# Optimization experiments

Hardware: AMD Instinct MI355X
Metric: run time of the kernel (lower is better)

The kernel has to match this reference:

```python
import jax, jax.numpy as jnp
import numpy as np

T = 2048      # time steps (X.shape[0])
D = 64        # input_dim (= future_dim)
H = 1024      # hidden_dim
OUT = 64      # output_dim
ND = 3        # num_decoders


def setup_inputs() -> dict:
    key = jax.random.key(0)
    ks = jax.random.split(key, 20)
    def p(k, shape, scale=0.03):
        return jax.random.normal(k, shape, dtype=jnp.float32) * scale
    return {
        "X": jax.random.normal(ks[0], (T, D), dtype=jnp.float32),
        # enc LSTMCell: input = fusion_dim = 2*D
        "enc_Wih": p(ks[1], (4 * H, 2 * D)), "enc_Whh": p(ks[2], (4 * H, H)),
        "enc_bih": p(ks[3], (4 * H,)), "enc_bhh": p(ks[4], (4 * H,)),
        # dec LSTMCell: input = H
        "dec_Wih": p(ks[5], (4 * H, H)), "dec_Whh": p(ks[6], (4 * H, H)),
        "dec_bih": p(ks[7], (4 * H,)), "dec_bhh": p(ks[8], (4 * H,)),
        # fc_relu heads
        "hx_W": p(ks[9], (H, H)), "hx_b": p(ks[10], (H,)),
        "cx_W": p(ks[11], (H, H)), "cx_b": p(ks[12], (H,)),
        "fus_W": p(ks[13], (H, OUT)), "fus_b": p(ks[14], (H,)),
        "fut_W": p(ks[15], (D, H)), "fut_b": p(ks[16], (D,)),
        # classifier (shared by encoder and decoder)
        "cls_W": p(ks[17], (OUT, H)), "cls_b": p(ks[18], (OUT,)),
    }


def _lstm_cell(x, h, c, Wih, Whh, bih, bhh):
    # torch.nn.LSTMCell gate order: i, f, g, o
    g = x @ Wih.T + bih + h @ Whh.T + bhh
    i, f, gg, o = jnp.split(g, 4, axis=-1)
    c_new = jax.nn.sigmoid(f) * c + jax.nn.sigmoid(i) * jnp.tanh(gg)
    h_new = jax.nn.sigmoid(o) * jnp.tanh(c_new)
    return h_new, c_new


def reference(X, enc_Wih, enc_Whh, enc_bih, enc_bhh,
              dec_Wih, dec_Whh, dec_bih, dec_bhh,
              hx_W, hx_b, cx_W, cx_b, fus_W, fus_b,
              fut_W, fut_b, cls_W, cls_b):
    relu = jax.nn.relu

    def step(carry, x_t):
        enc_hx, enc_cx, fut = carry  # [H], [H], [D]
        fusion = jnp.concatenate([x_t, fut])  # [2D]
        enc_hx, enc_cx = _lstm_cell(fusion, enc_hx, enc_cx,
                                    enc_Wih, enc_Whh, enc_bih, enc_bhh)
        enc_score = enc_hx @ cls_W.T + cls_b  # [OUT]
        dhx = relu(enc_hx @ hx_W.T + hx_b)
        dcx = relu(enc_cx @ cx_W.T + cx_b)
        fusion_in = jnp.zeros((H,), X.dtype)
        fut_new = jnp.zeros((D,), X.dtype)
        dscores = []
        for _ in range(ND):
            # Original bug preserved: decoder returns the UNCHANGED cx
            # (`decc_cx` typo), so dcx is never updated inside this loop.
            dhx, _unused_cx = _lstm_cell(fusion_in, dhx, dcx,
                                         dec_Wih, dec_Whh, dec_bih, dec_bhh)
            ds = dhx @ cls_W.T + cls_b
            dscores.append(ds)
            fusion_in = relu(ds @ fus_W.T + fus_b)
            fut_new = fut_new + relu(dhx @ fut_W.T + fut_b)
        fut_new = fut_new / ND
        return (enc_hx, enc_cx, fut_new), (enc_score, jnp.stack(dscores))

    init = (jnp.zeros((H,), X.dtype), jnp.zeros((H,), X.dtype),
            jnp.zeros((D,), X.dtype))
    _, (enc_scores, dec_scores) = jax.lax.scan(step, init, X[: T - ND])
    # enc_scores: [T-ND, OUT]; dec_scores: [T-ND, ND, OUT] -> [(T-ND)*ND, OUT]
    return enc_scores, dec_scores.reshape(-1, OUT)
```

## Files before the change

### kernel.cpp

```cpp
#include <hip/hip_runtime.h>
#include <hip/hip_bf16.h>


typedef unsigned short u16t;
typedef unsigned int u32t;
typedef unsigned long long u64t;

#define TSTEPS 2045
#define NWG 256
#define NTHR 512
#define SPINCAP 8192

#define HENC  0
#define CENC  4096
#define DHX   8192
#define DD1   12288
#define DD2   16384
#define SFF   20480
#define PARTF 22016

struct Params {
  const void *X, *eWih, *eWhh, *ebih, *ebhh, *dWih, *dWhh, *dbih, *dbhh,
             *hxW, *hxb, *cxW, *cxb, *fusW, *fusb_g, *futW, *futb_g, *clsW, *clsb_g;
  float* ws;
  void* out;
};

struct SharedMem {
  alignas(16) float encW[16 * 1152];
  alignas(16) u16t  decW[16 * 2048];
  alignas(16) float xs[2048];
  float cls_sl[256], fut_sl[256];
  float clsb[64], futb[64], fut_acc[64], dsbuf[64], fv3[64];
  float bias_e[16], bias_d[16], g16[16];
  float h4[4], dcx_s[4], encc[4], hxb4[4], cxb4[4];
  int bail;
  int badcnt;
};

__device__ __forceinline__ float bfu(u16t u){
  union { u32t i; float f; } v; v.i = ((u32t)u) << 16; return v.f;
}
__device__ __forceinline__ u32t fbits(float f){
  union { float f; u32t u; } c; c.f = f; return c.u;
}
__device__ __forceinline__ u16t bf16bits(float v){
  __hip_bfloat16 b = __float2bfloat16(v);
  union { __hip_bfloat16 b; u16t u; } c; c.b = b; return c.u;
}
template<bool F32>
__device__ __forceinline__ float ldE(const void* p, int i){
  if (F32) return ((const float*)p)[i];
  return bfu(((const u16t*)p)[i]);
}
template<bool F32>
__device__ __forceinline__ u16t ldB(const void* p, int i){
  if (F32) return bf16bits(((const float*)p)[i]);
  return ((const u16t*)p)[i];
}
template<bool F32>
__device__ __forceinline__ void stO(void* p, int i, float v){
  if (F32) ((float*)p)[i] = v;
  else     ((u16t*)p)[i] = bf16bits(v);
}
__device__ __forceinline__ float sigm(float x){ return 1.f / (1.f + __expf(-x)); }
__device__ __forceinline__ float tanhx(float x){
  float e = __expf(-2.f * fabsf(x));
  float t = (1.f - e) / (1.f + e);
  return copysignf(t, x);
}
__device__ __forceinline__ void stp(float* rowbase, int idx, float v, u32t ep){
  u64t u = (u64t)fbits(v) | ((u64t)ep << 32);
  __hip_atomic_store((u64t*)rowbase + idx, u,
                     __ATOMIC_RELAXED, __HIP_MEMORY_SCOPE_AGENT);
}
__device__ __forceinline__ float4 ld4c(const float* p){
  float4 r;
  asm volatile("global_load_dwordx4 %0, %1, off sc0 sc1\n\t"
               "s_waitcnt vmcnt(0)"
               : "=&v"(r) : "v"(p) : "memory");
  return r;
}
__device__ __forceinline__ void ld4c4(const float* p0, const float* p1,
                                      const float* p2, const float* p3,
                                      float4& r0, float4& r1, float4& r2, float4& r3){
  asm volatile(
    "global_load_dwordx4 %0, %4, off sc0 sc1\n\t"
    "global_load_dwordx4 %1, %5, off sc0 sc1\n\t"
    "global_load_dwordx4 %2, %6, off sc0 sc1\n\t"
    "global_load_dwordx4 %3, %7, off sc0 sc1\n\t"
    "s_waitcnt vmcnt(0)"
    : "=&v"(r0), "=&v"(r1), "=&v"(r2), "=&v"(r3)
    : "v"(p0), "v"(p1), "v"(p2), "v"(p3)
    : "memory");
}
__device__ __forceinline__ float2 poll2(const float* q, u32t ep, int* bail){
  float4 r; int sp = 0;
  for (;;){
    r = ld4c(q);
    if (fbits(r.y) == ep && fbits(r.w) == ep) break;
    if (*bail) break;
    if (++sp > SPINCAP){ *bail = 1; break; }
  }
  return float2{r.x, r.z};
}

template<bool F32>
__device__ __forceinline__ float hw_dot(const void* wbase, long off,
                                        const float* __restrict__ x,
                                        int K, int lane){
  float acc = 0.f;
  if (F32){
    const float* w = (const float*)wbase + off;
    for (int c = lane * 4; c < K; c += 128){
      float4 wv = *(const float4*)(w + c);
      float4 xv = *(const float4*)(x + c);
      acc = fmaf(wv.x, xv.x, acc); acc = fmaf(wv.y, xv.y, acc);
      acc = fmaf(wv.z, xv.z, acc); acc = fmaf(wv.w, xv.w, acc);
    }
  } else {
    const u16t* w = (const u16t*)wbase + off;
    for (int c = lane * 4; c < K; c += 128){
      ushort4 wv = *(const ushort4*)(w + c);
      float4  xv = *(const float4*)(x + c);
      acc = fmaf(bfu(wv.x), xv.x, acc); acc = fmaf(bfu(wv.y), xv.y, acc);
      acc = fmaf(bfu(wv.z), xv.z, acc); acc = fmaf(bfu(wv.w), xv.w, acc);
    }
  }
  #pragma unroll
  for (int o = 16; o; o >>= 1) acc += __shfl_xor(acc, o, 64);
  return acc;
}

__device__ __forceinline__ float lds_dot_f32(const float* __restrict__ w,
                                             const float* __restrict__ x,
                                             int K, int lane){
  float acc = 0.f;
  for (int c = lane * 4; c < K; c += 128){
    float4 wv = *(const float4*)(w + c);
    float4 xv = *(const float4*)(x + c);
    acc = fmaf(wv.x, xv.x, acc); acc = fmaf(wv.y, xv.y, acc);
    acc = fmaf(wv.z, xv.z, acc); acc = fmaf(wv.w, xv.w, acc);
  }
  #pragma unroll
  for (int o = 16; o; o >>= 1) acc += __shfl_xor(acc, o, 64);
  return acc;
}

__device__ __forceinline__ float lds_dot_bf16(const u16t* __restrict__ w,
                                              const float* __restrict__ x,
                                              int K, int lane){
  float acc = 0.f;
  for (int c = lane * 8; c < K; c += 256){
    uint4  wv = *(const uint4*)(w + c);
    float4 x0 = *(const float4*)(x + c);
    float4 x1 = *(const float4*)(x + c + 4);
    acc = fmaf(bfu((u16t)(wv.x & 0xffff)), x0.x, acc);
    acc = fmaf(bfu((u16t)(wv.x >> 16)),    x0.y, acc);
    acc = fmaf(bfu((u16t)(wv.y & 0xffff)), x0.z, acc);
    acc = fmaf(bfu((u16t)(wv.y >> 16)),    x0.w, acc);
    acc = fmaf(bfu((u16t)(wv.z & 0xffff)), x1.x, acc);
    acc = fmaf(bfu((u16t)(wv.z >> 16)),    x1.y, acc);
    acc = fmaf(bfu((u16t)(wv.w & 0xffff)), x1.z, acc);
    acc = fmaf(bfu((u16t)(wv.w >> 16)),    x1.w, acc);
  }
  #pragma unroll
  for (int o = 16; o; o >>= 1) acc += __shfl_xor(acc, o, 64);
  return acc;
}

template<bool F32>
__device__ __forceinline__ void reduce_phase(float* ws, int ph, int par, u32t ep,
                                             int t, SharedMem& S, void* out,
                                             int w, int hw, int lane){
  const int o = (w & 7) * 16 + hw;
  const float* row = ws + PARTF + (size_t)((par * 3 + ph) * 128 + o) * 512;
  const float* q = row + lane * 16;
  float4 r0, r1, r2, r3; int sp = 0;
  for (;;){
    ld4c4(q, q + 4, q + 8, q + 12, r0, r1, r2, r3);
    if (fbits(r0.y) == ep && fbits(r0.w) == ep && fbits(r1.y) == ep &&
        fbits(r1.w) == ep && fbits(r2.y) == ep && fbits(r2.w) == ep &&
        fbits(r3.y) == ep && fbits(r3.w) == ep) break;
    if (S.bail) break;
    if (++sp > SPINCAP){ S.bail = 1; break; }
  }
  float s = r0.x + r0.z + r1.x + r1.z + r2.x + r2.z + r3.x + r3.z;
  #pragma unroll
  for (int m = 16; m; m >>= 1) s += __shfl_xor(s, m, 64);
  if (lane == 0){
    float* sf = ws + SFF + (par * 3 + ph) * 256;
    if (o < 64){
      float v = s + S.clsb[o];
      stO<F32>(out, TSTEPS * 64 + (t * 3 + ph) * 64 + o, v);
      if (ph < 2) stp(sf, o, v, ep);
    } else {
      float v = fmaxf(s + S.futb[o - 64], 0.f);
      stp(sf, o, v, ep);
    }
  }
}

template<bool F32>
__device__ void run(const Params& p, SharedMem& S){
  const int tid  = threadIdx.x;
  const int w    = blockIdx.x;
  const int hw   = tid >> 5;
  const int lane = tid & 31;
  const long grow = (long)((hw >> 2) * 1024 + 4 * w + (hw & 3));
  float* ws = p.ws;

  {
    float* er = S.encW + hw * 1152;
    for (int c = lane; c < 128; c += 32)  er[c]       = ldE<F32>(p.eWih, (int)(grow * 128 + c));
    for (int c = lane; c < 1024; c += 32) er[128 + c] = ldE<F32>(p.eWhh, (int)(grow * 1024 + c));
    u16t* dr = S.decW + hw * 2048;
    for (int c = lane; c < 1024; c += 32){
      dr[c]        = ldB<F32>(p.dWih, (int)(grow * 1024 + c));
      dr[1024 + c] = ldB<F32>(p.dWhh, (int)(grow * 1024 + c));
    }
  }
  u32t fw[64];
  float fusb0, fusb1;
  {
    int h0 = 2 * tid, h1 = 2 * tid + 1;
    #pragma unroll
    for (int o = 0; o < 64; ++o){
      u16t lo = ldB<F32>(p.fusW, h0 * 64 + o);
      u16t hi = ldB<F32>(p.fusW, h1 * 64 + o);
      fw[o] = ((u32t)hi << 16) | lo;
    }
    fusb0 = ldE<F32>(p.fusb_g, h0);
    fusb1 = ldE<F32>(p.fusb_g, h1);
  }
  if (tid < 256){
    int o = tid >> 2, j = tid & 3;
    S.cls_sl[tid] = ldE<F32>(p.clsW, o * 1024 + 4 * w + j);
    S.fut_sl[tid] = ldE<F32>(p.futW, o * 1024 + 4 * w + j);
  }
  if (tid < 64){
    S.clsb[tid] = ldE<F32>(p.clsb_g, tid);
    S.futb[tid] = ldE<F32>(p.futb_g, tid);
    S.fut_acc[tid] = 0.f;
  }
  if (tid < 16){
    int gr = (tid >> 2) * 1024 + 4 * w + (tid & 3);
    S.bias_e[tid] = ldE<F32>(p.ebih, gr) + ldE<F32>(p.ebhh, gr);
    S.bias_d[tid] = ldE<F32>(p.dbih, gr) + ldE<F32>(p.dbhh, gr);
  }
  if (tid < 4){
    S.hxb4[tid] = ldE<F32>(p.hxb, 4 * w + tid);
    S.cxb4[tid] = ldE<F32>(p.cxb, 4 * w + tid);
    S.encc[tid] = 0.f;
  }
  __syncthreads();

  for (int t = 0; t < TSTEPS; ++t){
    const int  par  = t & 1;
    const int  ppar = par ^ 1;
    const u32t ep   = (u32t)(t + 1);
    const u32t epv  = (u32t)t;

    if (t > 0){
      if (tid < 32){
        const float* base = ws + SFF + (ppar * 3 + 2) * 256;
        float2 v = poll2(base + (32 + tid) * 4, epv, &S.bail);
        S.fv3[2 * tid] = v.x; S.fv3[2 * tid + 1] = v.y;
      }
      float2 v = poll2(ws + HENC + ppar * 2048 + tid * 4, epv, &S.bail);
      S.xs[128 + 2 * tid] = v.x; S.xs[129 + 2 * tid] = v.y;
    } else {
      S.xs[128 + 2 * tid] = 0.f; S.xs[129 + 2 * tid] = 0.f;
    }
    __syncthreads();
    if (tid < 64){
      S.xs[tid] = ldE<F32>(p.X, t * 64 + tid);
      float fv = (t > 0) ? (S.fut_acc[tid] + S.fv3[tid]) * (1.f / 3.f) : 0.f;
      S.xs[64 + tid] = fv;
      S.fut_acc[tid] = 0.f;
    }
    __syncthreads();
    {
      float a = lds_dot_f32(S.encW + hw * 1152, S.xs, 1152, lane) + S.bias_e[hw];
      if (lane == 0) S.g16[hw] = a;
    }
    __syncthreads();
    if (tid < 4){
      float gi = sigm(S.g16[tid]), gf = sigm(S.g16[4 + tid]),
            gg = tanhx(S.g16[8 + tid]), go = sigm(S.g16[12 + tid]);
      float c = gf * S.encc[tid] + gi * gg;
      float h = go * tanhx(c);
      S.encc[tid] = c;
      stp(ws + HENC + par * 2048, 4 * w + tid, h, ep);
      stp(ws + CENC + par * 2048, 4 * w + tid, c, ep);
    }

    {
      float2 v = poll2(ws + HENC + par * 2048 + tid * 4, ep, &S.bail);
      S.xs[2 * tid] = v.x; S.xs[2 * tid + 1] = v.y;
      float2 c = poll2(ws + CENC + par * 2048 + tid * 4, ep, &S.bail);
      S.xs[1024 + 2 * tid] = c.x; S.xs[1025 + 2 * tid] = c.y;
    }
    __syncthreads();
    if (hw < 4){
      float d = fmaxf(hw_dot<F32>(p.hxW, (long)(4 * w + hw) * 1024, S.xs, 1024, lane)
                      + S.hxb4[hw], 0.f);
      if (lane == 0) stp(ws + DHX + par * 2048, 4 * w + hw, d, ep);
    } else if (hw < 8){
      int j = hw - 4;
      float d = fmaxf(hw_dot<F32>(p.cxW, (long)(4 * w + j) * 1024, S.xs + 1024, 1024, lane)
                      + S.cxb4[j], 0.f);
      if (lane == 0) S.dcx_s[j] = d;
    } else if (w >= 8 && w < 16){
      int r = (w - 8) * 8 + (hw - 8);
      float s = hw_dot<F32>(p.clsW, (long)r * 1024, S.xs, 1024, lane) + S.clsb[r];
      if (lane == 0) stO<F32>(p.out, t * 64 + r, s);
    }

    {
      float2 v = poll2(ws + DHX + par * 2048 + tid * 4, ep, &S.bail);
      S.xs[2 * tid] = v.x; S.xs[2 * tid + 1] = v.y;
    }
    __syncthreads();
    {
      float a = lds_dot_bf16(S.decW + hw * 2048 + 1024, S.xs, 1024, lane) + S.bias_d[hw];
      if (lane == 0) S.g16[hw] = a;
    }
    __syncthreads();
    if (tid < 4){
      float gi = sigm(S.g16[tid]), gf = sigm(S.g16[4 + tid]),
            gg = tanhx(S.g16[8 + tid]), go = sigm(S.g16[12 + tid]);
      float c = gf * S.dcx_s[tid] + gi * gg;
      float h = go * tanhx(c);
      S.h4[tid] = h;
      stp(ws + DD1 + par * 2048, 4 * w + tid, h, ep);
    }
    __syncthreads();
    if (tid < 64){
      float sv = 0.f, fv = 0.f;
      #pragma unroll
      for (int j = 0; j < 4; ++j){
        sv = fmaf(S.cls_sl[tid * 4 + j], S.h4[j], sv);
        fv = fmaf(S.fut_sl[tid * 4 + j], S.h4[j], fv);
      }
      float* base = ws + PARTF + (size_t)((par * 3 + 0) * 128) * 512;
      stp(base + (size_t)tid * 512,        w, sv, ep);
      stp(base + (size_t)(64 + tid) * 512, w, fv, ep);
    }

    for (int di = 2; di <= 3; ++di){
      const int ph = di - 2;
      if (w >= 16 + ph * 8 && w < 24 + ph * 8)
        reduce_phase<F32>(ws, ph, par, ep, t, S, p.out, w, hw, lane);
      {
        const float* dbuf = ws + (di == 2 ? DD1 : DD2) + par * 2048;
        float2 v = poll2(dbuf + tid * 4, ep, &S.bail);
        S.xs[1024 + 2 * tid] = v.x; S.xs[1025 + 2 * tid] = v.y;
      }
      __syncthreads();
      float accA = lds_dot_bf16(S.decW + hw * 2048 + 1024, S.xs + 1024, 1024, lane);
      if (tid < 64){
        const float* sf = ws + SFF + (par * 3 + ph) * 256;
        float2 v = poll2(sf + tid * 4, ep, &S.bail);
        if (tid < 32){ S.dsbuf[2 * tid] = v.x; S.dsbuf[2 * tid + 1] = v.y; }
        else { S.fv3[2 * (tid - 32)] = v.x; S.fv3[2 * (tid - 32) + 1] = v.y; }
      }
      __syncthreads();
      if (tid < 64) S.fut_acc[tid] += S.fv3[tid];
      {
        float a0 = fusb0, a1 = fusb1;
        #pragma unroll
        for (int o = 0; o < 64; ++o){
          float d = S.dsbuf[o];
          a0 = fmaf(bfu((u16t)(fw[o] & 0xffff)), d, a0);
          a1 = fmaf(bfu((u16t)(fw[o] >> 16)),    d, a1);
        }
        S.xs[2 * tid]     = fmaxf(a0, 0.f);
        S.xs[2 * tid + 1] = fmaxf(a1, 0.f);
      }
      __syncthreads();
      float accB = lds_dot_bf16(S.decW + hw * 2048, S.xs, 1024, lane);
      {
        float a = accA + accB + S.bias_d[hw];
        if (lane == 0) S.g16[hw] = a;
      }
      __syncthreads();
      if (tid < 4){
        float gi = sigm(S.g16[tid]), gf = sigm(S.g16[4 + tid]),
              gg = tanhx(S.g16[8 + tid]), go = sigm(S.g16[12 + tid]);
        float c = gf * S.dcx_s[tid] + gi * gg;
        float h = go * tanhx(c);
        S.h4[tid] = h;
        if (di == 2) stp(ws + DD2 + par * 2048, 4 * w + tid, h, ep);
      }
      __syncthreads();
      if (tid < 64){
        float sv = 0.f, fv = 0.f;
        #pragma unroll
        for (int j = 0; j < 4; ++j){
          sv = fmaf(S.cls_sl[tid * 4 + j], S.h4[j], sv);
          fv = fmaf(S.fut_sl[tid * 4 + j], S.h4[j], fv);
        }
        float* base = ws + PARTF + (size_t)((par * 3 + di - 1) * 128) * 512;
        stp(base + (size_t)tid * 512,        w, sv, ep);
        stp(base + (size_t)(64 + tid) * 512, w, fv, ep);
      }
    }
    if (w >= 32 && w < 40)
      reduce_phase<F32>(ws, 2, par, ep, t, S, p.out, w, hw, lane);
  }
}

__global__ __launch_bounds__(NTHR, 2)
void trn_persist(Params p){
  __shared__ SharedMem S;
  if (threadIdx.x == 0){ S.bail = 0; S.badcnt = 0; }
  __syncthreads();
  if (threadIdx.x < 256){
    u16t u = ((const u16t*)p.X)[threadIdx.x];
    int e = (u >> 7) & 0xff;
    if (e == 0 || e >= 141) atomicAdd(&S.badcnt, 1);
  }
  __syncthreads();
  if (S.badcnt >= 3) run<true>(p, S);
  else               run<false>(p, S);
}

extern "C" void kernel_launch(void* const* d_in, const int* in_sizes, int n_in,
                              void* d_out, int out_size, void* d_ws, size_t ws_size,
                              hipStream_t stream){
  Params P;
  P.X      = d_in[0];
  P.eWih   = d_in[1];
  P.eWhh   = d_in[2];
  P.ebih   = d_in[3];
  P.ebhh   = d_in[4];
  P.dWih   = d_in[5];
  P.dWhh   = d_in[6];
  P.dbih   = d_in[7];
  P.dbhh   = d_in[8];
  P.hxW    = d_in[9];
  P.hxb    = d_in[10];
  P.cxW    = d_in[11];
  P.cxb    = d_in[12];
  P.fusW   = d_in[13];
  P.fusb_g = d_in[14];
  P.futW   = d_in[15];
  P.futb_g = d_in[16];
  P.clsW   = d_in[17];
  P.clsb_g = d_in[18];
  P.ws     = (float*)d_ws;
  P.out    = d_out;

  void* args[] = { &P };
  hipLaunchCooperativeKernel((void*)trn_persist, dim3(NWG), dim3(NTHR),
                             args, 0, stream);
}
```

Baseline: 53.63 ms.

## Replace epoch-tagged partial reduction with global atomic-add accumulators and counters

```diff
diff --git a/kernel.cpp b/kernel.cpp
--- a/kernel.cpp
+++ b/kernel.cpp
@@ -10,14 +10,17 @@
 #define NWG 256
 #define NTHR 512
 #define SPINCAP 8192
+#define MAGIC 0x5a5a5a5aU
 
 #define HENC  0
 #define CENC  4096
 #define DHX   8192
 #define DD1   12288
 #define DD2   16384
-#define SFF   20480
-#define PARTF 22016
+#define ACCF  20480
+#define CNTF  45056
+#define BARF  45248
+#define ZTOT  24768
 
 struct Params {
   const void *X, *eWih, *eWhh, *ebih, *ebhh, *dWih, *dWhh, *dbih, *dbhh,
@@ -30,10 +33,12 @@
   alignas(16) float encW[16 * 1152];
   alignas(16) u16t  decW[16 * 2048];
   alignas(16) float xs[2048];
+  alignas(16) float hprev[1024];
+  alignas(16) float xsf[128];
   float cls_sl[256], fut_sl[256];
-  float clsb[64], futb[64], fut_acc[64], dsbuf[64], fv3[64];
+  float clsb[64], futb[64], fut_acc[64], dsbuf[64], xnext[64];
   float bias_e[16], bias_d[16], g16[16];
-  float h4[4], dcx_s[4], encc[4], hxb4[4], cxb4[4];
+  float dcx_s[4], encc[4], hxb4[4], cxb4[4];
   int bail;
   int badcnt;
 };
@@ -73,6 +78,9 @@
   u64t u = (u64t)fbits(v) | ((u64t)ep << 32);
   __hip_atomic_store((u64t*)rowbase + idx, u,
                      __ATOMIC_RELAXED, __HIP_MEMORY_SCOPE_AGENT);
+}
+__device__ __forceinline__ void stu32(u32t* p, u32t v){
+  __hip_atomic_store(p, v, __ATOMIC_RELAXED, __HIP_MEMORY_SCOPE_AGENT);
 }
 __device__ __forceinline__ float4 ld4c(const float* p){
   float4 r;
@@ -81,18 +89,35 @@
                : "=&v"(r) : "v"(p) : "memory");
   return r;
 }
-__device__ __forceinline__ void ld4c4(const float* p0, const float* p1,
-                                      const float* p2, const float* p3,
-                                      float4& r0, float4& r1, float4& r2, float4& r3){
+__device__ __forceinline__ uint4 ld4cu4(const u32t* p){
+  uint4 r;
+  asm volatile("global_load_dwordx4 %0, %1, off sc0 sc1\n\t"
+               "s_waitcnt vmcnt(0)"
+               : "=&v"(r) : "v"(p) : "memory");
+  return r;
+}
+__device__ __forceinline__ u32t ld1cu(const u32t* p){
+  u32t r;
+  asm volatile("global_load_dword %0, %1, off sc0 sc1\n\t"
+               "s_waitcnt vmcnt(0)"
+               : "=&v"(r) : "v"(p) : "memory");
+  return r;
+}
+__device__ __forceinline__ void ld4c2(const float* p0, const float* p1,
+                                      float4& a, float4& b){
   asm volatile(
-    "global_load_dwordx4 %0, %4, off sc0 sc1\n\t"
-    "global_load_dwordx4 %1, %5, off sc0 sc1\n\t"
-    "global_load_dwordx4 %2, %6, off sc0 sc1\n\t"
-    "global_load_dwordx4 %3, %7, off sc0 sc1\n\t"
+    "global_load_dwordx4 %0, %2, off sc0 sc1\n\t"
+    "global_load_dwordx4 %1, %3, off sc0 sc1\n\t"
     "s_waitcnt vmcnt(0)"
-    : "=&v"(r0), "=&v"(r1), "=&v"(r2), "=&v"(r3)
-    : "v"(p0), "v"(p1), "v"(p2), "v"(p3)
+    : "=&v"(a), "=&v"(b)
+    : "v"(p0), "v"(p1)
     : "memory");
+}
+__device__ __forceinline__ void gadd_f32(float* p, float v){
+  asm volatile("global_atomic_add_f32 %0, %1, off sc1" :: "v"(p), "v"(v) : "memory");
+}
+__device__ __forceinline__ void gadd_u32(u32t* p, u32t v){
+  asm volatile("global_atomic_add %0, %1, off sc1" :: "v"(p), "v"(v) : "memory");
 }
 __device__ __forceinline__ float2 poll2(const float* q, u32t ep, int* bail){
   float4 r; int sp = 0;
@@ -132,9 +157,9 @@
   return acc;
 }
 
-__device__ __forceinline__ float lds_dot_f32(const float* __restrict__ w,
-                                             const float* __restrict__ x,
-                                             int K, int lane){
+__device__ __forceinline__ float dotnr_f32(const float* __restrict__ w,
+                                           const float* __restrict__ x,
+                                           int K, int lane){
   float acc = 0.f;
   for (int c = lane * 4; c < K; c += 128){
     float4 wv = *(const float4*)(w + c);
@@ -142,14 +167,11 @@
     acc = fmaf(wv.x, xv.x, acc); acc = fmaf(wv.y, xv.y, acc);
     acc = fmaf(wv.z, xv.z, acc); acc = fmaf(wv.w, xv.w, acc);
   }
-  #pragma unroll
-  for (int o = 16; o; o >>= 1) acc += __shfl_xor(acc, o, 64);
   return acc;
 }
-
-__device__ __forceinline__ float lds_dot_bf16(const u16t* __restrict__ w,
-                                              const float* __restrict__ x,
-                                              int K, int lane){
+__device__ __forceinline__ float dotnr_bf16(const u16t* __restrict__ w,
+                                            const float* __restrict__ x,
+                                            int K, int lane){
   float acc = 0.f;
   for (int c = lane * 8; c < K; c += 256){
     uint4  wv = *(const uint4*)(w + c);
@@ -164,41 +186,46 @@
     acc = fmaf(bfu((u16t)(wv.w & 0xffff)), x1.z, acc);
     acc = fmaf(bfu((u16t)(wv.w >> 16)),    x1.w, acc);
   }
+  return acc;
+}
+__device__ __forceinline__ float wred(float a){
   #pragma unroll
-  for (int o = 16; o; o >>= 1) acc += __shfl_xor(acc, o, 64);
-  return acc;
-}
-
-template<bool F32>
-__device__ __forceinline__ void reduce_phase(float* ws, int ph, int par, u32t ep,
-                                             int t, SharedMem& S, void* out,
-                                             int w, int hw, int lane){
-  const int o = (w & 7) * 16 + hw;
-  const float* row = ws + PARTF + (size_t)((par * 3 + ph) * 128 + o) * 512;
-  const float* q = row + lane * 16;
-  float4 r0, r1, r2, r3; int sp = 0;
+  for (int o = 16; o; o >>= 1) a += __shfl_xor(a, o, 64);
+  return a;
+}
+
+__device__ __forceinline__ void partial_adds(float* ws, u32t* wsu, int rot, int ph,
+                                             const SharedMem& S, int tid, int w,
+                                             float hval){
+  float h0 = __shfl(hval, 0, 64), h1 = __shfl(hval, 1, 64),
+        h2 = __shfl(hval, 2, 64), h3 = __shfl(hval, 3, 64);
+  const float* cs = S.cls_sl + tid * 4;
+  const float* fs = S.fut_sl + tid * 4;
+  float sv = cs[0]*h0 + cs[1]*h1 + cs[2]*h2 + cs[3]*h3;
+  float fv = fs[0]*h0 + fs[1]*h1 + fs[2]*h2 + fs[3]*h3;
+  float* bb = ws + ACCF + (size_t)(((rot * 3 + ph) * 128 + tid) * 16 + (w & 3));
+  gadd_f32(bb, sv);
+  gadd_f32(bb + 1024, fv);
+  asm volatile("s_waitcnt vmcnt(0)" ::: "memory");
+  if (tid == 0) gadd_u32(wsu + CNTF + (rot * 3 + ph) * 16 + (w & 3), 1u);
+}
+
+__device__ __forceinline__ void sf_consume(float* ws, const u32t* wsu, int rot, int ph,
+                                           SharedMem& S, int tid,
+                                           float& dsv, float& fv){
+  const u32t* cp = wsu + CNTF + (rot * 3 + ph) * 16;
+  int sp = 0;
   for (;;){
-    ld4c4(q, q + 4, q + 8, q + 12, r0, r1, r2, r3);
-    if (fbits(r0.y) == ep && fbits(r0.w) == ep && fbits(r1.y) == ep &&
-        fbits(r1.w) == ep && fbits(r2.y) == ep && fbits(r2.w) == ep &&
-        fbits(r3.y) == ep && fbits(r3.w) == ep) break;
+    uint4 c = ld4cu4(cp);
+    if (c.x + c.y + c.z + c.w == 256u) break;
     if (S.bail) break;
     if (++sp > SPINCAP){ S.bail = 1; break; }
   }
-  float s = r0.x + r0.z + r1.x + r1.z + r2.x + r2.z + r3.x + r3.z;
-  #pragma unroll
-  for (int m = 16; m; m >>= 1) s += __shfl_xor(s, m, 64);
-  if (lane == 0){
-    float* sf = ws + SFF + (par * 3 + ph) * 256;
-    if (o < 64){
-      float v = s + S.clsb[o];
-      stO<F32>(out, TSTEPS * 64 + (t * 3 + ph) * 64 + o, v);
-      if (ph < 2) stp(sf, o, v, ep);
-    } else {
-      float v = fmaxf(s + S.futb[o - 64], 0.f);
-      stp(sf, o, v, ep);
-    }
-  }
+  const float* ap = ws + ACCF + (size_t)((rot * 3 + ph) * 128 + tid) * 16;
+  float4 a, b;
+  ld4c2(ap, ap + 1024, a, b);
+  dsv = a.x + a.y + a.z + a.w + S.clsb[tid];
+  fv  = fmaxf(b.x + b.y + b.z + b.w + S.futb[tid], 0.f);
 }
 
 template<bool F32>
@@ -209,6 +236,26 @@
   const int lane = tid & 31;
   const long grow = (long)((hw >> 2) * 1024 + 4 * w + (hw & 3));
   float* ws = p.ws;
+  u32t* wsu = (u32t*)p.ws;
+
+  for (int i = w * NTHR + tid; i < ZTOT; i += NWG * NTHR)
+    stu32(wsu + ACCF + i, 0u);
+  asm volatile("s_waitcnt vmcnt(0)" ::: "memory");
+  __syncthreads();
+  if (tid == 0) stu32(wsu + BARF + w, MAGIC);
+  if (w == 0){
+    if (tid < NWG){
+      int sp = 0;
+      while (ld1cu(wsu + BARF + tid) != MAGIC && ++sp < (1 << 22)) {}
+    }
+    __syncthreads();
+    if (tid == 0) stu32(wsu + BARF + NWG, MAGIC);
+  }
+  if (tid == 0){
+    int sp = 0;
+    while (ld1cu(wsu + BARF + NWG) != MAGIC && ++sp < (1 << 22)) {}
+  }
+  __syncthreads();
 
   {
     float* er = S.encW + hw * 1152;
@@ -243,6 +290,7 @@
     S.futb[tid] = ldE<F32>(p.futb_g, tid);
     S.fut_acc[tid] = 0.f;
   }
+  S.hprev[2 * tid] = 0.f; S.hprev[2 * tid + 1] = 0.f;
   if (tid < 16){
     int gr = (tid >> 2) * 1024 + 4 * w + (tid & 3);
     S.bias_e[tid] = ldE<F32>(p.ebih, gr) + ldE<F32>(p.ebhh, gr);
@@ -256,32 +304,28 @@
   __syncthreads();
 
   for (int t = 0; t < TSTEPS; ++t){
-    const int  par  = t & 1;
-    const int  ppar = par ^ 1;
-    const u32t ep   = (u32t)(t + 1);
-    const u32t epv  = (u32t)t;
-
-    if (t > 0){
-      if (tid < 32){
-        const float* base = ws + SFF + (ppar * 3 + 2) * 256;
-        float2 v = poll2(base + (32 + tid) * 4, epv, &S.bail);
-        S.fv3[2 * tid] = v.x; S.fv3[2 * tid + 1] = v.y;
-      }
-      float2 v = poll2(ws + HENC + ppar * 2048 + tid * 4, epv, &S.bail);
-      S.xs[128 + 2 * tid] = v.x; S.xs[129 + 2 * tid] = v.y;
-    } else {
-      S.xs[128 + 2 * tid] = 0.f; S.xs[129 + 2 * tid] = 0.f;
-    }
-    __syncthreads();
+    const int  par = t & 1;
+    const int  rot = t & 3;
+    const u32t ep  = (u32t)(t + 1);
+
     if (tid < 64){
-      S.xs[tid] = ldE<F32>(p.X, t * 64 + tid);
-      float fv = (t > 0) ? (S.fut_acc[tid] + S.fv3[tid]) * (1.f / 3.f) : 0.f;
-      S.xs[64 + tid] = fv;
-      S.fut_acc[tid] = 0.f;
+      float xv = (t == 0) ? ldE<F32>(p.X, tid) : S.xnext[tid];
+      float futv = 0.f;
+      if (t > 0){
+        float dsv, fv;
+        sf_consume(ws, wsu, (t - 1) & 3, 2, S, tid, dsv, fv);
+        futv = (S.fut_acc[tid] + fv) * (1.f / 3.f);
+        S.fut_acc[tid] = 0.f;
+        if (w == 10) stO<F32>(p.out, TSTEPS * 64 + ((t - 1) * 3 + 2) * 64 + tid, dsv);
+      }
+      S.xsf[tid] = xv;
+      S.xsf[64 + tid] = futv;
     }
     __syncthreads();
     {
-      float a = lds_dot_f32(S.encW + hw * 1152, S.xs, 1152, lane) + S.bias_e[hw];
+      float a = dotnr_f32(S.encW + hw * 1152, S.xsf, 128, lane)
+              + dotnr_f32(S.encW + hw * 1152 + 128, S.hprev, 1024, lane);
+      a = wred(a) + S.bias_e[hw];
       if (lane == 0) S.g16[hw] = a;
     }
     __syncthreads();
@@ -296,10 +340,19 @@
     }
 
     {
-      float2 v = poll2(ws + HENC + par * 2048 + tid * 4, ep, &S.bail);
-      S.xs[2 * tid] = v.x; S.xs[2 * tid + 1] = v.y;
-      float2 c = poll2(ws + CENC + par * 2048 + tid * 4, ep, &S.bail);
-      S.xs[1024 + 2 * tid] = c.x; S.xs[1025 + 2 * tid] = c.y;
+      const float* ph_ = ws + HENC + par * 2048 + tid * 4;
+      const float* pc_ = ws + CENC + par * 2048 + tid * 4;
+      float4 a, b; int sp = 0;
+      for (;;){
+        ld4c2(ph_, pc_, a, b);
+        if (fbits(a.y) == ep && fbits(a.w) == ep &&
+            fbits(b.y) == ep && fbits(b.w) == ep) break;
+        if (S.bail) break;
+        if (++sp > SPINCAP){ S.bail = 1; break; }
+      }
+      S.xs[2 * tid] = a.x;        S.xs[2 * tid + 1] = a.z;
+      S.hprev[2 * tid] = a.x;     S.hprev[2 * tid + 1] = a.z;
+      S.xs[1024 + 2 * tid] = b.x; S.xs[1025 + 2 * tid] = b.z;
     }
     __syncthreads();
     if (hw < 4){
@@ -316,6 +369,7 @@
       float s = hw_dot<F32>(p.clsW, (long)r * 1024, S.xs, 1024, lane) + S.clsb[r];
       if (lane == 0) stO<F32>(p.out, t * 64 + r, s);
     }
+    __syncthreads();
 
     {
       float2 v = poll2(ws + DHX + par * 2048 + tid * 4, ep, &S.bail);
@@ -323,50 +377,48 @@
     }
     __syncthreads();
     {
-      float a = lds_dot_bf16(S.decW + hw * 2048 + 1024, S.xs, 1024, lane) + S.bias_d[hw];
+      float a = wred(dotnr_bf16(S.decW + hw * 2048 + 1024, S.xs, 1024, lane)) + S.bias_d[hw];
       if (lane == 0) S.g16[hw] = a;
     }
     __syncthreads();
-    if (tid < 4){
-      float gi = sigm(S.g16[tid]), gf = sigm(S.g16[4 + tid]),
-            gg = tanhx(S.g16[8 + tid]), go = sigm(S.g16[12 + tid]);
-      float c = gf * S.dcx_s[tid] + gi * gg;
-      float h = go * tanhx(c);
-      S.h4[tid] = h;
-      stp(ws + DD1 + par * 2048, 4 * w + tid, h, ep);
-    }
-    __syncthreads();
-    if (tid < 64){
-      float sv = 0.f, fv = 0.f;
-      #pragma unroll
-      for (int j = 0; j < 4; ++j){
-        sv = fmaf(S.cls_sl[tid * 4 + j], S.h4[j], sv);
-        fv = fmaf(S.fut_sl[tid * 4 + j], S.h4[j], fv);
-      }
-      float* base = ws + PARTF + (size_t)((par * 3 + 0) * 128) * 512;
-      stp(base + (size_t)tid * 512,        w, sv, ep);
-      stp(base + (size_t)(64 + tid) * 512, w, fv, ep);
+    {
+      float hval = 0.f;
+      if (tid < 4){
+        float gi = sigm(S.g16[tid]), gf = sigm(S.g16[4 + tid]),
+              gg = tanhx(S.g16[8 + tid]), go = sigm(S.g16[12 + tid]);
+        float c = gf * S.dcx_s[tid] + gi * gg;
+        hval = go * tanhx(c);
+        stp(ws + DD1 + par * 2048, 4 * w + tid, hval, ep);
+      }
+      if (tid < 64){
+        partial_adds(ws, wsu, rot, 0, S, tid, w, hval);
+        S.xnext[tid] = ldE<F32>(p.X, (t + 1) * 64 + tid);
+      }
+    }
+    if (w >= 40 && w < 48){
+      const int r2 = (t + 2) & 3;
+      for (int i = (w - 40) * NTHR + tid; i < 6144; i += 8 * NTHR)
+        stu32(wsu + ACCF + r2 * 6144 + i, 0u);
+      if (w == 40 && tid < 48) stu32(wsu + CNTF + r2 * 48 + tid, 0u);
+      asm volatile("s_waitcnt vmcnt(0)" ::: "memory");
     }
 
     for (int di = 2; di <= 3; ++di){
       const int ph = di - 2;
-      if (w >= 16 + ph * 8 && w < 24 + ph * 8)
-        reduce_phase<F32>(ws, ph, par, ep, t, S, p.out, w, hw, lane);
       {
-        const float* dbuf = ws + (di == 2 ? DD1 : DD2) + par * 2048;
-        float2 v = poll2(dbuf + tid * 4, ep, &S.bail);
+        float2 v = poll2(ws + (di == 2 ? DD1 : DD2) + par * 2048 + tid * 4, ep, &S.bail);
         S.xs[1024 + 2 * tid] = v.x; S.xs[1025 + 2 * tid] = v.y;
       }
       __syncthreads();
-      float accA = lds_dot_bf16(S.decW + hw * 2048 + 1024, S.xs + 1024, 1024, lane);
+      float accA = dotnr_bf16(S.decW + hw * 2048 + 1024, S.xs + 1024, 1024, lane);
       if (tid < 64){
-        const float* sf = ws + SFF + (par * 3 + ph) * 256;
-        float2 v = poll2(sf + tid * 4, ep, &S.bail);
-        if (tid < 32){ S.dsbuf[2 * tid] = v.x; S.dsbuf[2 * tid + 1] = v.y; }
-        else { S.fv3[2 * (tid - 32)] = v.x; S.fv3[2 * (tid - 32) + 1] = v.y; }
+        float dsv, fv;
+        sf_consume(ws, wsu, rot, ph, S, tid, dsv, fv);
+        S.dsbuf[tid] = dsv;
+        S.fut_acc[tid] += fv;
+        if (w == 8 + ph) stO<F32>(p.out, TSTEPS * 64 + (t * 3 + ph) * 64 + tid, dsv);
       }
       __syncthreads();
-      if (tid < 64) S.fut_acc[tid] += S.fv3[tid];
       {
         float a0 = fusb0, a1 = fusb1;
         #pragma unroll
@@ -379,35 +431,30 @@
         S.xs[2 * tid + 1] = fmaxf(a1, 0.f);
       }
       __syncthreads();
-      float accB = lds_dot_bf16(S.decW + hw * 2048, S.xs, 1024, lane);
       {
-        float a = accA + accB + S.bias_d[hw];
+        float a = wred(accA + dotnr_bf16(S.decW + hw * 2048, S.xs, 1024, lane))
+                + S.bias_d[hw];
         if (lane == 0) S.g16[hw] = a;
       }
       __syncthreads();
-      if (tid < 4){
-        float gi = sigm(S.g16[tid]), gf = sigm(S.g16[4 + tid]),
-              gg = tanhx(S.g16[8 + tid]), go = sigm(S.g16[12 + tid]);
-        float c = gf * S.dcx_s[tid] + gi * gg;
-        float h = go * tanhx(c);
-        S.h4[tid] = h;
-        if (di == 2) stp(ws + DD2 + par * 2048, 4 * w + tid, h, ep);
-      }
-      __syncthreads();
-      if (tid < 64){
-        float sv = 0.f, fv = 0.f;
-        #pragma unroll
-        for (int j = 0; j < 4; ++j){
-          sv = fmaf(S.cls_sl[tid * 4 + j], S.h4[j], sv);
-          fv = fmaf(S.fut_sl[tid * 4 + j], S.h4[j], fv);
+      {
+        float hval = 0.f;
+        if (tid < 4){
+          float gi = sigm(S.g16[tid]), gf = sigm(S.g16[4 + tid]),
+                gg = tanhx(S.g16[8 + tid]), go = sigm(S.g16[12 + tid]);
+          float c = gf * S.dcx_s[tid] + gi * gg;
+          hval = go * tanhx(c);
+          if (di == 2) stp(ws + DD2 + par * 2048, 4 * w + tid, hval, ep);
         }
-        float* base = ws + PARTF + (size_t)((par * 3 + di - 1) * 128) * 512;
-        stp(base + (size_t)tid * 512,        w, sv, ep);
-        stp(base + (size_t)(64 + tid) * 512, w, fv, ep);
-      }
-    }
-    if (w >= 32 && w < 40)
-      reduce_phase<F32>(ws, 2, par, ep, t, S, p.out, w, hw, lane);
+        if (tid < 64) partial_adds(ws, wsu, rot, di - 1, S, tid, w, hval);
+      }
+    }
+  }
+
+  if (w == 10 && tid < 64){
+    float dsv, fv;
+    sf_consume(ws, wsu, (TSTEPS - 1) & 3, 2, S, tid, dsv, fv);
+    stO<F32>(p.out, TSTEPS * 64 + ((TSTEPS - 1) * 3 + 2) * 64 + tid, dsv);
   }
 }
 
```

Result: slower. 91.58 ms (+70.8%).

## Precompute encoder recurrent dot early and merge h/c polling

Applied to the files above, without the earlier changes.

```diff
diff --git a/kernel.cpp b/kernel.cpp
--- a/kernel.cpp
+++ b/kernel.cpp
@@ -30,8 +30,9 @@
   alignas(16) float encW[16 * 1152];
   alignas(16) u16t  decW[16 * 2048];
   alignas(16) float xs[2048];
+  alignas(16) float xsf[128];
   float cls_sl[256], fut_sl[256];
-  float clsb[64], futb[64], fut_acc[64], dsbuf[64], fv3[64];
+  float clsb[64], futb[64], fut_acc[64], dsbuf[64], fv3[64], xnext[64];
   float bias_e[16], bias_d[16], g16[16];
   float h4[4], dcx_s[4], encc[4], hxb4[4], cxb4[4];
   int bail;
@@ -80,6 +81,16 @@
                "s_waitcnt vmcnt(0)"
                : "=&v"(r) : "v"(p) : "memory");
   return r;
+}
+__device__ __forceinline__ void ld4c2(const float* p0, const float* p1,
+                                      float4& a, float4& b){
+  asm volatile(
+    "global_load_dwordx4 %0, %2, off sc0 sc1\n\t"
+    "global_load_dwordx4 %1, %3, off sc0 sc1\n\t"
+    "s_waitcnt vmcnt(0)"
+    : "=&v"(a), "=&v"(b)
+    : "v"(p0), "v"(p1)
+    : "memory");
 }
 __device__ __forceinline__ void ld4c4(const float* p0, const float* p1,
                                       const float* p2, const float* p3,
@@ -132,9 +143,9 @@
   return acc;
 }
 
-__device__ __forceinline__ float lds_dot_f32(const float* __restrict__ w,
-                                             const float* __restrict__ x,
-                                             int K, int lane){
+__device__ __forceinline__ float dotnr_f32(const float* __restrict__ w,
+                                           const float* __restrict__ x,
+                                           int K, int lane){
   float acc = 0.f;
   for (int c = lane * 4; c < K; c += 128){
     float4 wv = *(const float4*)(w + c);
@@ -142,9 +153,12 @@
     acc = fmaf(wv.x, xv.x, acc); acc = fmaf(wv.y, xv.y, acc);
     acc = fmaf(wv.z, xv.z, acc); acc = fmaf(wv.w, xv.w, acc);
   }
+  return acc;
+}
+__device__ __forceinline__ float wred(float a){
   #pragma unroll
-  for (int o = 16; o; o >>= 1) acc += __shfl_xor(acc, o, 64);
-  return acc;
+  for (int o = 16; o; o >>= 1) a += __shfl_xor(a, o, 64);
+  return a;
 }
 
 __device__ __forceinline__ float lds_dot_bf16(const u16t* __restrict__ w,
@@ -253,6 +267,7 @@
     S.cxb4[tid] = ldE<F32>(p.cxb, 4 * w + tid);
     S.encc[tid] = 0.f;
   }
+  float enc_pre = 0.f;
   __syncthreads();
 
   for (int t = 0; t < TSTEPS; ++t){
@@ -261,27 +276,22 @@
     const u32t ep   = (u32t)(t + 1);
     const u32t epv  = (u32t)t;
 
-    if (t > 0){
-      if (tid < 32){
-        const float* base = ws + SFF + (ppar * 3 + 2) * 256;
-        float2 v = poll2(base + (32 + tid) * 4, epv, &S.bail);
-        S.fv3[2 * tid] = v.x; S.fv3[2 * tid + 1] = v.y;
-      }
-      float2 v = poll2(ws + HENC + ppar * 2048 + tid * 4, epv, &S.bail);
-      S.xs[128 + 2 * tid] = v.x; S.xs[129 + 2 * tid] = v.y;
-    } else {
-      S.xs[128 + 2 * tid] = 0.f; S.xs[129 + 2 * tid] = 0.f;
+    if (t > 0 && tid < 32){
+      const float* base = ws + SFF + (ppar * 3 + 2) * 256;
+      float2 v = poll2(base + (32 + tid) * 4, epv, &S.bail);
+      S.fv3[2 * tid] = v.x; S.fv3[2 * tid + 1] = v.y;
     }
     __syncthreads();
     if (tid < 64){
-      S.xs[tid] = ldE<F32>(p.X, t * 64 + tid);
+      S.xsf[tid] = (t == 0) ? ldE<F32>(p.X, tid) : S.xnext[tid];
       float fv = (t > 0) ? (S.fut_acc[tid] + S.fv3[tid]) * (1.f / 3.f) : 0.f;
-      S.xs[64 + tid] = fv;
+      S.xsf[64 + tid] = fv;
       S.fut_acc[tid] = 0.f;
     }
     __syncthreads();
     {
-      float a = lds_dot_f32(S.encW + hw * 1152, S.xs, 1152, lane) + S.bias_e[hw];
+      float a = wred(enc_pre + dotnr_f32(S.encW + hw * 1152, S.xsf, 128, lane))
+              + S.bias_e[hw];
       if (lane == 0) S.g16[hw] = a;
     }
     __syncthreads();
@@ -296,10 +306,18 @@
     }
 
     {
-      float2 v = poll2(ws + HENC + par * 2048 + tid * 4, ep, &S.bail);
-      S.xs[2 * tid] = v.x; S.xs[2 * tid + 1] = v.y;
-      float2 c = poll2(ws + CENC + par * 2048 + tid * 4, ep, &S.bail);
-      S.xs[1024 + 2 * tid] = c.x; S.xs[1025 + 2 * tid] = c.y;
+      const float* ph_ = ws + HENC + par * 2048 + tid * 4;
+      const float* pc_ = ws + CENC + par * 2048 + tid * 4;
+      float4 a, b; int sp = 0;
+      for (;;){
+        ld4c2(ph_, pc_, a, b);
+        if (fbits(a.y) == ep && fbits(a.w) == ep &&
+            fbits(b.y) == ep && fbits(b.w) == ep) break;
+        if (S.bail) break;
+        if (++sp > SPINCAP){ S.bail = 1; break; }
+      }
+      S.xs[2 * tid] = a.x;        S.xs[2 * tid + 1] = a.z;
+      S.xs[1024 + 2 * tid] = b.x; S.xs[1025 + 2 * tid] = b.z;
     }
     __syncthreads();
     if (hw < 4){
@@ -316,6 +334,8 @@
       float s = hw_dot<F32>(p.clsW, (long)r * 1024, S.xs, 1024, lane) + S.clsb[r];
       if (lane == 0) stO<F32>(p.out, t * 64 + r, s);
     }
+    enc_pre = dotnr_f32(S.encW + hw * 1152 + 128, S.xs, 1024, lane);
+    __syncthreads();
 
     {
       float2 v = poll2(ws + DHX + par * 2048 + tid * 4, ep, &S.bail);
@@ -346,12 +366,11 @@
       float* base = ws + PARTF + (size_t)((par * 3 + 0) * 128) * 512;
       stp(base + (size_t)tid * 512,        w, sv, ep);
       stp(base + (size_t)(64 + tid) * 512, w, fv, ep);
+      S.xnext[tid] = ldE<F32>(p.X, (t + 1) * 64 + tid);
     }
 
     for (int di = 2; di <= 3; ++di){
       const int ph = di - 2;
-      if (w >= 16 + ph * 8 && w < 24 + ph * 8)
-        reduce_phase<F32>(ws, ph, par, ep, t, S, p.out, w, hw, lane);
       {
         const float* dbuf = ws + (di == 2 ? DD1 : DD2) + par * 2048;
         float2 v = poll2(dbuf + tid * 4, ep, &S.bail);
@@ -359,6 +378,8 @@
       }
       __syncthreads();
       float accA = lds_dot_bf16(S.decW + hw * 2048 + 1024, S.xs + 1024, 1024, lane);
+      if (w >= 16 + ph * 8 && w < 24 + ph * 8)
+        reduce_phase<F32>(ws, ph, par, ep, t, S, p.out, w, hw, lane);
       if (tid < 64){
         const float* sf = ws + SFF + (par * 3 + ph) * 256;
         float2 v = poll2(sf + tid * 4, ep, &S.bail);
```

Result: slower. 57.37 ms (+7.0%).
